# Kernel tuning notes

Hardware: AMD Instinct MI355X
Metric: run time of the kernel (lower is better)

Reference implementation:

```python
import jax, jax.numpy as jnp
import numpy as np


def conv2d(x, w, b, stride=1, pad=0):
    out = jax.lax.conv_general_dilated(
        x, w, (stride, stride), ((pad, pad), (pad, pad)),
        dimension_numbers=('NCHW', 'OIHW', 'NCHW'))
    return out + b[None, :, None, None]


def maxpool2(x):
    return jax.lax.reduce_window(x, -jnp.inf, jax.lax.max,
                                 (1, 1, 2, 2), (1, 1, 2, 2), 'VALID')


def pixel_match_(x, y):
    # x, y: (1, C, H, W). 9-way shifted squared-diff cost volume.
    _, C, H, W = x.shape
    yc = y[0, :, 1:H - 1, 1:W - 1]
    inner = []
    for dh in range(3):
        for dw in range(3):
            tmp = x[0, :, dh:dh + H - 2, dw:dw + W - 2] - yc
            inner.append(jnp.sum(tmp * tmp, axis=0))
    inner = jnp.stack(inner)  # (9, H-2, W-2)
    diff = jnp.zeros((9, H, W), x.dtype).at[:, 1:H - 1, 1:W - 1].set(inner)
    diff = 1.0 / jnp.sqrt(diff + 0.01)
    diff = diff / jnp.sum(diff, axis=0, keepdims=True)
    return diff[None]  # (1, 9, H, W)


def positional(H, W, dtype):
    h = jnp.arange(H, dtype=dtype)
    w = jnp.arange(W, dtype=dtype)
    h = 2.0 * h / h[-1] - 1.0
    w = 2.0 * w / w[-1] - 1.0
    ph = jnp.broadcast_to(h[:, None], (H, W))
    pw = jnp.broadcast_to(w[None, :], (H, W))
    return jnp.stack([ph, pw])[None]  # (1, 2, H, W)


def pixel_match(x, y):
    return jnp.concatenate(
        [pixel_match_(x, y), pixel_match_(y, x),
         positional(x.shape[2], x.shape[3], x.dtype)], axis=1)


def adaptive_max_pool3(x):
    # torch adaptive_max_pool2d semantics: bin i spans [floor(i*H/3), ceil((i+1)*H/3))
    _, C, H, W = x.shape
    rows = []
    for i in range(3):
        hs, he = (i * H) // 3, -((-(i + 1) * H) // 3)
        cols = []
        for j in range(3):
            ws, we = (j * W) // 3, -((-(j + 1) * W) // 3)
            cols.append(jnp.max(x[:, :, hs:he, ws:we], axis=(2, 3)))
        rows.append(jnp.stack(cols, axis=-1))
    return jnp.stack(rows, axis=-2)  # (1, C, 3, 3)


def setup_inputs() -> dict:
    key = jax.random.key(0)
    ks = jax.random.split(key, 16)
    f = jnp.float32
    H = W = 1024
    s = 0.05
    return {
        'x1': jax.random.normal(ks[0], (3, H, W), f),
        'x2': jax.random.normal(ks[1], (3, H, W), f),
        'enc_w': jax.random.normal(ks[2], (24, 3, 3, 3), f) * s,
        'enc_b': jax.random.normal(ks[3], (24,), f) * s,
        'embed_w': jax.random.normal(ks[4], (32, 24, 1, 1), f) * s,
        'embed_b': jax.random.normal(ks[5], (32,), f) * s,
        'dense_w': jax.random.normal(ks[6], (8, 32, 5, 5), f) * s,
        'dense_b': jax.random.normal(ks[7], (8,), f) * s,
        'f1_w': jax.random.normal(ks[8], (64, 48, 1, 1), f) * s,
        'f1_b': jax.random.normal(ks[9], (64,), f) * s,
        'f2_w': jax.random.normal(ks[10], (128, 64, 3, 3), f) * s,
        'f2_b': jax.random.normal(ks[11], (128,), f) * s,
        'f3_w': jax.random.normal(ks[12], (6, 128), f) * s,
        'f3_b': jax.random.normal(ks[13], (6,), f) * s,
    }


def reference(x1, x2, enc_w, enc_b, embed_w, embed_b, dense_w, dense_b,
              f1_w, f1_b, f2_w, f2_b, f3_w, f3_b):
    def coding(x):
        x = x[None]  # (1,3,H,W)
        x = jax.lax.stop_gradient(conv2d(x, enc_w, enc_b, pad=1))  # frozen encoder
        x = conv2d(x, embed_w, embed_b)
        return maxpool2(x)

    c1 = coding(x1)
    c2 = coding(x2)
    level1 = maxpool2(pixel_match(c1, c2))
    p1 = maxpool2(c1)
    p2 = maxpool2(c2)
    level2 = pixel_match(p1, p2)
    dense = jax.nn.leaky_relu(conv2d(p1 - p2, dense_w, dense_b, pad=2))
    x = jnp.concatenate([level1, level2, dense], axis=1)  # (1,48,H/4,W/4)
    x = conv2d(x, f1_w, f1_b)
    x = adaptive_max_pool3(x)
    x = conv2d(x, f2_w, f2_b).reshape(1, 128)
    tmp = jnp.sum(x * x) + 0.001
    x = x / jnp.sqrt(tmp)
    x = (x @ f3_w.T + f3_b).reshape(2, 3)
    x = jnp.concatenate([x, jnp.zeros((1, 3), x.dtype)], axis=0)
    return jnp.eye(3, dtype=x.dtype) + jnp.clip(x, -0.11, 0.11) + x * 0.01
```

## Files before the change

### kernel.cpp

```cpp
#include <hip/hip_runtime.h>
#include <math.h>


__global__ void fuse_weights_kernel(const float* __restrict__ enc_w,
                                    const float* __restrict__ enc_b,
                                    const float* __restrict__ embed_w,
                                    const float* __restrict__ embed_b,
                                    float* __restrict__ weff_t,
                                    float* __restrict__ beff) {
    int t = threadIdx.x;
    for (int idx = t; idx < 27 * 32; idx += blockDim.x) {
        int r = idx >> 5, o = idx & 31;
        float s = 0.f;
        for (int k = 0; k < 24; ++k) s += embed_w[o * 24 + k] * enc_w[k * 27 + r];
        weff_t[idx] = s;
    }
    if (t < 32) {
        float s = embed_b[t];
        for (int k = 0; k < 24; ++k) s += embed_w[t * 24 + k] * enc_b[k];
        beff[t] = s;
    }
}

__global__ __launch_bounds__(256) void coding_kernel(
    const float* __restrict__ x1, const float* __restrict__ x2,
    const float* __restrict__ weff_t, const float* __restrict__ beff,
    float* __restrict__ c1, float* __restrict__ c2,
    float* __restrict__ p1, float* __restrict__ p2) {
    int tx = threadIdx.x, ty = threadIdx.y;
    int img = blockIdx.z;
    const float* x = img ? x2 : x1;
    float* c = img ? c2 : c1;
    float* p = img ? p2 : p1;
    int Y = blockIdx.y * 16 + ty;
    int cx = blockIdx.x * 16 + tx;
    int X0 = 2 * cx;
    bool interior = (blockIdx.y > 0 && blockIdx.y < 63 &&
                     blockIdx.x > 0 && blockIdx.x < 31);
    float acc0[32], acc1[32];
#pragma unroll
    for (int o = 0; o < 32; ++o) {
        acc0[o] = beff[o];
        acc1[o] = acc0[o];
    }
#pragma unroll 1
    for (int ci = 0; ci < 3; ++ci) {
        float in[3][4];
        const float* xc = x + ci * 1048576;
        if (interior) {
#pragma unroll
            for (int r = 0; r < 3; ++r) {
                const float* row = xc + (Y - 1 + r) * 1024 + X0 - 1;
#pragma unroll
                for (int q = 0; q < 4; ++q) in[r][q] = row[q];
            }
        } else {
#pragma unroll
            for (int r = 0; r < 3; ++r)
#pragma unroll
                for (int q = 0; q < 4; ++q) {
                    int gy = Y - 1 + r, gx = X0 - 1 + q;
                    in[r][q] = (gy >= 0 && gy < 1024 && gx >= 0 && gx < 1024)
                                   ? xc[gy * 1024 + gx]
                                   : 0.f;
                }
        }
#pragma unroll
        for (int ky = 0; ky < 3; ++ky)
#pragma unroll
            for (int kx = 0; kx < 3; ++kx) {
                const float* wrow = weff_t + (ci * 9 + ky * 3 + kx) * 32;
                float xa = in[ky][kx];
                float xb = in[ky][kx + 1];
#pragma unroll
                for (int o = 0; o < 32; ++o) {
                    float wv = wrow[o];
                    acc0[o] = fmaf(wv, xa, acc0[o]);
                    acc1[o] = fmaf(wv, xb, acc1[o]);
                }
            }
    }
#pragma unroll
    for (int o = 0; o < 32; ++o) {
        float m = fmaxf(acc0[o], acc1[o]);
        acc0[o] = fmaxf(m, __shfl_xor(m, 16, 64));
    }
    int cpix = (Y >> 1) * 512 + cx;
    if ((ty & 1) == 0) {
        float4* cd = (float4*)(c + cpix * 32);
#pragma unroll
        for (int q = 0; q < 8; ++q)
            cd[q] = make_float4(acc0[4 * q], acc0[4 * q + 1], acc0[4 * q + 2],
                                acc0[4 * q + 3]);
    }
#pragma unroll
    for (int o = 0; o < 32; ++o) {
        float v = fmaxf(acc0[o], __shfl_xor(acc0[o], 1, 64));
        acc0[o] = fmaxf(v, __shfl_xor(v, 32, 64));
    }
    if (((ty & 3) == 0) && ((tx & 1) == 0)) {
        int ppix = (Y >> 2) * 256 + (cx >> 1);
        float4* pd = (float4*)(p + ppix * 32);
#pragma unroll
        for (int q = 0; q < 8; ++q)
            pd[q] = make_float4(acc0[4 * q], acc0[4 * q + 1], acc0[4 * q + 2],
                                acc0[4 * q + 3]);
    }
}

__global__ __launch_bounds__(256) void pm512_pool_kernel(
    const float* __restrict__ c1, const float* __restrict__ c2,
    float* __restrict__ feat) {
    int tid = threadIdx.x;
    int quad = tid & 3;
    int pl = tid >> 2;
    int px = pl & 7, py = pl >> 3;
    int sw = blockIdx.x * 8 + px;
    int sh = blockIdx.y * 8 + py;
    bool interior = (sh >= 1 && sh <= 510 && sw >= 1 && sw <= 510);
    const float* b1 = c1 + (sh * 512 + sw) * 32 + quad * 8;
    const float* b2 = c2 + (sh * 512 + sw) * 32 + quad * 8;
    float a1[9], a2[9];
#pragma unroll
    for (int k = 0; k < 9; ++k) { a1[k] = 0.f; a2[k] = 0.f; }
    if (interior) {
        float4 y1a = ((const float4*)b1)[0], y1b = ((const float4*)b1)[1];
        float4 y2a = ((const float4*)b2)[0], y2b = ((const float4*)b2)[1];
#pragma unroll
        for (int dh = -1; dh <= 1; ++dh)
#pragma unroll
            for (int dw = -1; dw <= 1; ++dw) {
                int k = (dh + 1) * 3 + (dw + 1);
                const float4* n1 = (const float4*)(b1 + (dh * 512 + dw) * 32);
                const float4* n2 = (const float4*)(b2 + (dh * 512 + dw) * 32);
                float4 na = n1[0], nA = n1[1], nb = n2[0], nB = n2[1];
                float s1 = a1[k], s2 = a2[k], t;
                t = na.x - y2a.x; s1 = fmaf(t, t, s1);
                t = na.y - y2a.y; s1 = fmaf(t, t, s1);
                t = na.z - y2a.z; s1 = fmaf(t, t, s1);
                t = na.w - y2a.w; s1 = fmaf(t, t, s1);
                t = nA.x - y2b.x; s1 = fmaf(t, t, s1);
                t = nA.y - y2b.y; s1 = fmaf(t, t, s1);
                t = nA.z - y2b.z; s1 = fmaf(t, t, s1);
                t = nA.w - y2b.w; s1 = fmaf(t, t, s1);
                t = nb.x - y1a.x; s2 = fmaf(t, t, s2);
                t = nb.y - y1a.y; s2 = fmaf(t, t, s2);
                t = nb.z - y1a.z; s2 = fmaf(t, t, s2);
                t = nb.w - y1a.w; s2 = fmaf(t, t, s2);
                t = nB.x - y1b.x; s2 = fmaf(t, t, s2);
                t = nB.y - y1b.y; s2 = fmaf(t, t, s2);
                t = nB.z - y1b.z; s2 = fmaf(t, t, s2);
                t = nB.w - y1b.w; s2 = fmaf(t, t, s2);
                a1[k] = s1;
                a2[k] = s2;
            }
    }
#pragma unroll
    for (int k = 0; k < 9; ++k) {
        a1[k] += __shfl_xor(a1[k], 1, 64);
        a1[k] += __shfl_xor(a1[k], 2, 64);
        a2[k] += __shfl_xor(a2[k], 1, 64);
        a2[k] += __shfl_xor(a2[k], 2, 64);
    }
    float d[20];
    if (interior) {
        float s1 = 0.f, s2 = 0.f;
#pragma unroll
        for (int k = 0; k < 9; ++k) {
            a1[k] = 1.0f / sqrtf(a1[k] + 0.01f);
            a2[k] = 1.0f / sqrtf(a2[k] + 0.01f);
            s1 += a1[k];
            s2 += a2[k];
        }
        float i1 = 1.0f / s1, i2 = 1.0f / s2;
#pragma unroll
        for (int k = 0; k < 9; ++k) {
            d[k] = a1[k] * i1;
            d[9 + k] = a2[k] * i2;
        }
    } else {
#pragma unroll
        for (int k = 0; k < 18; ++k) d[k] = 1.0f / 9.0f;
    }
#pragma unroll
    for (int k = 0; k < 18; ++k) {
        float v = fmaxf(d[k], __shfl_xor(d[k], 4, 64));
        d[k] = fmaxf(v, __shfl_xor(v, 32, 64));
    }
    d[18] = 2.0f * (sh | 1) / 511.0f - 1.0f;
    d[19] = 2.0f * (sw | 1) / 511.0f - 1.0f;
    if ((tid & 36) == 0) {
        int opix = (sh >> 1) * 256 + (sw >> 1);
#pragma unroll
        for (int j = 0; j < 5; ++j)
            feat[(quad * 5 + j) * 65536 + opix] = d[quad * 5 + j];
    }
}

__global__ __launch_bounds__(256) void pm256_kernel(
    const float* __restrict__ p1, const float* __restrict__ p2,
    float* __restrict__ feat) {
    int tid = threadIdx.x;
    int quad = tid & 3;
    int pl = tid >> 2;
    int px = pl & 7, py = pl >> 3;
    int w = blockIdx.x * 8 + px;
    int h = blockIdx.y * 8 + py;
    bool interior = (h >= 1 && h <= 254 && w >= 1 && w <= 254);
    const float* b1 = p1 + (h * 256 + w) * 32 + quad * 8;
    const float* b2 = p2 + (h * 256 + w) * 32 + quad * 8;
    float a1[9], a2[9];
#pragma unroll
    for (int k = 0; k < 9; ++k) { a1[k] = 0.f; a2[k] = 0.f; }
    if (interior) {
        float4 y1a = ((const float4*)b1)[0], y1b = ((const float4*)b1)[1];
        float4 y2a = ((const float4*)b2)[0], y2b = ((const float4*)b2)[1];
#pragma unroll
        for (int dh = -1; dh <= 1; ++dh)
#pragma unroll
            for (int dw = -1; dw <= 1; ++dw) {
                int k = (dh + 1) * 3 + (dw + 1);
                const float4* n1 = (const float4*)(b1 + (dh * 256 + dw) * 32);
                const float4* n2 = (const float4*)(b2 + (dh * 256 + dw) * 32);
                float4 na = n1[0], nA = n1[1], nb = n2[0], nB = n2[1];
                float s1 = a1[k], s2 = a2[k], t;
                t = na.x - y2a.x; s1 = fmaf(t, t, s1);
                t = na.y - y2a.y; s1 = fmaf(t, t, s1);
                t = na.z - y2a.z; s1 = fmaf(t, t, s1);
                t = na.w - y2a.w; s1 = fmaf(t, t, s1);
                t = nA.x - y2b.x; s1 = fmaf(t, t, s1);
                t = nA.y - y2b.y; s1 = fmaf(t, t, s1);
                t = nA.z - y2b.z; s1 = fmaf(t, t, s1);
                t = nA.w - y2b.w; s1 = fmaf(t, t, s1);
                t = nb.x - y1a.x; s2 = fmaf(t, t, s2);
                t = nb.y - y1a.y; s2 = fmaf(t, t, s2);
                t = nb.z - y1a.z; s2 = fmaf(t, t, s2);
                t = nb.w - y1a.w; s2 = fmaf(t, t, s2);
                t = nB.x - y1b.x; s2 = fmaf(t, t, s2);
                t = nB.y - y1b.y; s2 = fmaf(t, t, s2);
                t = nB.z - y1b.z; s2 = fmaf(t, t, s2);
                t = nB.w - y1b.w; s2 = fmaf(t, t, s2);
                a1[k] = s1;
                a2[k] = s2;
            }
    }
#pragma unroll
    for (int k = 0; k < 9; ++k) {
        a1[k] += __shfl_xor(a1[k], 1, 64);
        a1[k] += __shfl_xor(a1[k], 2, 64);
        a2[k] += __shfl_xor(a2[k], 1, 64);
        a2[k] += __shfl_xor(a2[k], 2, 64);
    }
    float d[20];
    if (interior) {
        float s1 = 0.f, s2 = 0.f;
#pragma unroll
        for (int k = 0; k < 9; ++k) {
            a1[k] = 1.0f / sqrtf(a1[k] + 0.01f);
            a2[k] = 1.0f / sqrtf(a2[k] + 0.01f);
            s1 += a1[k];
            s2 += a2[k];
        }
        float i1 = 1.0f / s1, i2 = 1.0f / s2;
#pragma unroll
        for (int k = 0; k < 9; ++k) {
            d[k] = a1[k] * i1;
            d[9 + k] = a2[k] * i2;
        }
    } else {
#pragma unroll
        for (int k = 0; k < 18; ++k) d[k] = 1.0f / 9.0f;
    }
    d[18] = 2.0f * h / 255.0f - 1.0f;
    d[19] = 2.0f * w / 255.0f - 1.0f;
    int pix = h * 256 + w;
#pragma unroll
    for (int j = 0; j < 5; ++j)
        feat[(20 + quad * 5 + j) * 65536 + pix] = d[quad * 5 + j];
}

__global__ __launch_bounds__(256) void dense_part_kernel(
    const float* __restrict__ p1, const float* __restrict__ p2,
    const float* __restrict__ dw, float* __restrict__ part) {
    __shared__ float sdiff[4 * 1296];
    __shared__ float sw[4 * 8 * 28];
    int tx = threadIdx.x, ty = threadIdx.y;
    int tid = ty * 16 + tx;
    int bz = blockIdx.z;
    int h0 = blockIdx.y * 32, w0 = blockIdx.x * 32;
    for (int idx = tid; idx < 1296; idx += 256) {
        int yy = idx / 36, xx = idx % 36;
        int gy = h0 + yy - 2, gx = w0 + xx - 2;
        float4 dv = make_float4(0.f, 0.f, 0.f, 0.f);
        if (gy >= 0 && gy < 256 && gx >= 0 && gx < 256) {
            const float4* q1 =
                (const float4*)(p1 + (gy * 256 + gx) * 32 + bz * 4);
            const float4* q2 =
                (const float4*)(p2 + (gy * 256 + gx) * 32 + bz * 4);
            float4 v1 = q1[0], v2 = q2[0];
            dv = make_float4(v1.x - v2.x, v1.y - v2.y, v1.z - v2.z, v1.w - v2.w);
        }
        sdiff[0 * 1296 + idx] = dv.x;
        sdiff[1 * 1296 + idx] = dv.y;
        sdiff[2 * 1296 + idx] = dv.z;
        sdiff[3 * 1296 + idx] = dv.w;
    }
    for (int idx = tid; idx < 4 * 8 * 28; idx += 256) {
        int ci = idx / 224, r = idx % 224;
        int o = r / 28, k = r % 28;
        sw[idx] = (k < 25) ? dw[o * 800 + (bz * 4 + ci) * 25 + k] : 0.f;
    }
    __syncthreads();
    float acc[4][8];
#pragma unroll
    for (int pq = 0; pq < 4; ++pq)
#pragma unroll
        for (int o = 0; o < 8; ++o) acc[pq][o] = 0.f;
    for (int ci = 0; ci < 4; ++ci) {
        float patch[6][6];
#pragma unroll
        for (int yy = 0; yy < 6; ++yy) {
            const float* rowp = &sdiff[ci * 1296 + (2 * ty + yy) * 36 + 2 * tx];
#pragma unroll
            for (int cpair = 0; cpair < 3; ++cpair) {
                float2 lp = *(const float2*)&rowp[2 * cpair];
                patch[yy][2 * cpair] = lp.x;
                patch[yy][2 * cpair + 1] = lp.y;
            }
        }
#pragma unroll
        for (int o = 0; o < 8; ++o) {
            float wreg[28];
            const float4* wp = (const float4*)&sw[(ci * 8 + o) * 28];
#pragma unroll
            for (int q = 0; q < 7; ++q) {
                float4 wv = wp[q];
                wreg[4 * q] = wv.x;
                wreg[4 * q + 1] = wv.y;
                wreg[4 * q + 2] = wv.z;
                wreg[4 * q + 3] = wv.w;
            }
#pragma unroll
            for (int ky = 0; ky < 5; ++ky)
#pragma unroll
                for (int kx = 0; kx < 5; ++kx) {
                    float wv = wreg[ky * 5 + kx];
#pragma unroll
                    for (int pq = 0; pq < 4; ++pq)
                        acc[pq][o] = fmaf(
                            wv, patch[ky + (pq >> 1)][kx + (pq & 1)], acc[pq][o]);
                }
        }
    }
#pragma unroll
    for (int pq = 0; pq < 4; ++pq) {
        int h = h0 + 2 * ty + (pq >> 1), w = w0 + 2 * tx + (pq & 1);
        int pix = h * 256 + w;
#pragma unroll
        for (int o = 0; o < 8; ++o)
            part[bz * 524288 + o * 65536 + pix] = acc[pq][o];
    }
}

__global__ __launch_bounds__(256) void dense_reduce_kernel(
    const float* __restrict__ part, const float* __restrict__ db,
    float* __restrict__ feat) {
    int idx = blockIdx.x * 256 + threadIdx.x;
    int o = idx >> 16;
    float s = db[o];
#pragma unroll
    for (int z = 0; z < 8; ++z) s += part[z * 524288 + idx];
    float v = (s >= 0.f) ? s : 0.01f * s;
    feat[40 * 65536 + idx] = v;
}

__global__ __launch_bounds__(256) void f1_kernel(
    const float* __restrict__ feat, const float* __restrict__ f1w,
    const float* __restrict__ f1b, float* __restrict__ out) {
    __shared__ float sw[1536];
    __shared__ float sb[32];
    int og = blockIdx.y;
    int tid = threadIdx.x;
    for (int i = tid; i < 1536; i += 256) sw[i] = f1w[og * 1536 + i];
    if (tid < 32) sb[tid] = f1b[og * 32 + tid];
    __syncthreads();
    int pix = blockIdx.x * 256 + tid;
    float f[48];
#pragma unroll
    for (int c = 0; c < 48; ++c) f[c] = feat[c * 65536 + pix];
#pragma unroll
    for (int o = 0; o < 32; ++o) {
        float a = sb[o];
        const float4* wv = (const float4*)&sw[o * 48];
#pragma unroll
        for (int c4 = 0; c4 < 12; ++c4) {
            float4 ww = wv[c4];
            a = fmaf(ww.x, f[c4 * 4], a);
            a = fmaf(ww.y, f[c4 * 4 + 1], a);
            a = fmaf(ww.z, f[c4 * 4 + 2], a);
            a = fmaf(ww.w, f[c4 * 4 + 3], a);
        }
        out[(og * 32 + o) * 65536 + pix] = a;
    }
}

__global__ __launch_bounds__(256) void pool3_kernel(
    const float* __restrict__ f1out, float* __restrict__ pooled) {
    int b = blockIdx.x;
    int c = b / 9, ij = b % 9, i = ij / 3, j = ij % 3;
    int hs = (i * 256) / 3, he = ((i + 1) * 256 + 2) / 3;
    int ws = (j * 256) / 3, we = ((j + 1) * 256 + 2) / 3;
    const float* src = f1out + c * 65536;
    int nh = he - hs, nw = we - ws, tot = nh * nw;
    float m = -INFINITY;
    for (int t = threadIdx.x; t < tot; t += 256) {
        int r = t / nw, q = t - r * nw;
        m = fmaxf(m, src[(hs + r) * 256 + (ws + q)]);
    }
    for (int off = 32; off > 0; off >>= 1) m = fmaxf(m, __shfl_down(m, off, 64));
    __shared__ float red[4];
    if ((threadIdx.x & 63) == 0) red[threadIdx.x >> 6] = m;
    __syncthreads();
    if (threadIdx.x == 0)
        pooled[b] = fmaxf(fmaxf(red[0], red[1]), fmaxf(red[2], red[3]));
}

__global__ __launch_bounds__(128) void final_kernel(
    const float* __restrict__ pooled, const float* __restrict__ f2w,
    const float* __restrict__ f2b, const float* __restrict__ f3w,
    const float* __restrict__ f3b, float* __restrict__ out) {
    __shared__ float xn[128];
    __shared__ float red[2];
    __shared__ float ov[6];
    int t = threadIdx.x;
    float a = f2b[t];
    for (int c = 0; c < 64; ++c)
#pragma unroll
        for (int k = 0; k < 9; ++k)
            a = fmaf(f2w[t * 576 + c * 9 + k], pooled[c * 9 + k], a);
    float sq = a * a;
    for (int off = 32; off > 0; off >>= 1) sq += __shfl_down(sq, off, 64);
    if ((t & 63) == 0) red[t >> 6] = sq;
    __syncthreads();
    float tmp = red[0] + red[1] + 0.001f;
    float scale = 1.0f / sqrtf(tmp);
    xn[t] = a * scale;
    __syncthreads();
    if (t < 6) {
        float o = f3b[t];
        for (int k = 0; k < 128; ++k) o = fmaf(f3w[t * 128 + k], xn[k], o);
        ov[t] = o;
    }
    __syncthreads();
    if (t < 9) {
        int r = t / 3, cc = t % 3;
        float v = 0.f;
        if (r < 2) {
            float x = ov[r * 3 + cc];
            float cl = fminf(fmaxf(x, -0.11f), 0.11f);
            v = cl + 0.01f * x;
        }
        if (r == cc) v += 1.0f;
        out[t] = v;
    }
}

extern "C" void kernel_launch(void* const* d_in, const int* in_sizes, int n_in,
                              void* d_out, int out_size, void* d_ws,
                              size_t ws_size, hipStream_t stream) {
    const float* x1 = (const float*)d_in[0];
    const float* x2 = (const float*)d_in[1];
    const float* enc_w = (const float*)d_in[2];
    const float* enc_b = (const float*)d_in[3];
    const float* embed_w = (const float*)d_in[4];
    const float* embed_b = (const float*)d_in[5];
    const float* dense_w = (const float*)d_in[6];
    const float* dense_b = (const float*)d_in[7];
    const float* f1_w = (const float*)d_in[8];
    const float* f1_b = (const float*)d_in[9];
    const float* f2_w = (const float*)d_in[10];
    const float* f2_b = (const float*)d_in[11];
    const float* f3_w = (const float*)d_in[12];
    const float* f3_b = (const float*)d_in[13];

    float* ws = (float*)d_ws;
    float* weff_t = ws;
    float* beff = ws + 864;
    float* c1 = ws + 1024;
    float* c2 = c1 + 8388608;
    float* p1 = c2 + 8388608;
    float* p2 = p1 + 2097152;
    float* feat = p2 + 2097152;
    float* pooled = feat + 3145728;
    float* f1o = c1;
    float* part = c2;

    fuse_weights_kernel<<<1, 256, 0, stream>>>(enc_w, enc_b, embed_w, embed_b,
                                               weff_t, beff);
    coding_kernel<<<dim3(32, 64, 2), dim3(16, 16), 0, stream>>>(
        x1, x2, weff_t, beff, c1, c2, p1, p2);
    pm512_pool_kernel<<<dim3(64, 64), 256, 0, stream>>>(c1, c2, feat);
    pm256_kernel<<<dim3(32, 32), 256, 0, stream>>>(p1, p2, feat);
    dense_part_kernel<<<dim3(8, 8, 8), dim3(16, 16), 0, stream>>>(
        p1, p2, dense_w, part);
    dense_reduce_kernel<<<2048, 256, 0, stream>>>(part, dense_b, feat);
    f1_kernel<<<dim3(256, 2), 256, 0, stream>>>(feat, f1_w, f1_b, f1o);
    pool3_kernel<<<576, 256, 0, stream>>>(f1o, pooled);
    final_kernel<<<1, 128, 0, stream>>>(pooled, f2_w, f2_b, f3_w, f3_b,
                                        (float*)d_out);
}
```

Measured before the change: 184.9 us.

## Split coding conv channels across lanes and read weights directly from global

The coding kernel now gives each pooled pixel to four lanes, each computing 8 output channels over a 2x2 window instead of 32 channels for two pixels. This cuts per-thread accumulator registers and lets each lane write contiguous float4 chunks without the first shuffle stage. The dense and f1 kernels drop their shared-memory weight staging and read the uniform weights straight from global memory, with rolled loops to limit code size and registers. This relies on scalar/constant caching of the weights and may raise the number of global loads per FMA.

Result: slower. 213.4 us (+15.4%).

```diff
diff --git a/kernel.cpp b/kernel.cpp
--- a/kernel.cpp
+++ b/kernel.cpp
@@ -27,39 +27,46 @@
     const float* __restrict__ weff_t, const float* __restrict__ beff,
     float* __restrict__ c1, float* __restrict__ c2,
     float* __restrict__ p1, float* __restrict__ p2) {
-    int tx = threadIdx.x, ty = threadIdx.y;
+    int tid = threadIdx.x;
+    int quad = tid & 3;
+    int pl = tid >> 2;
+    int px = pl & 7, py = pl >> 3;
     int img = blockIdx.z;
     const float* x = img ? x2 : x1;
     float* c = img ? c2 : c1;
     float* p = img ? p2 : p1;
-    int Y = blockIdx.y * 16 + ty;
-    int cx = blockIdx.x * 16 + tx;
-    int X0 = 2 * cx;
+    int cy = blockIdx.y * 8 + py;
+    int cx = blockIdx.x * 8 + px;
+    int Y0 = 2 * cy, X0 = 2 * cx;
     bool interior = (blockIdx.y > 0 && blockIdx.y < 63 &&
-                     blockIdx.x > 0 && blockIdx.x < 31);
-    float acc0[32], acc1[32];
-#pragma unroll
-    for (int o = 0; o < 32; ++o) {
-        acc0[o] = beff[o];
-        acc1[o] = acc0[o];
+                     blockIdx.x > 0 && blockIdx.x < 63);
+    float4 bb0 = *(const float4*)(beff + quad * 8);
+    float4 bb1 = *(const float4*)(beff + quad * 8 + 4);
+    float acc[4][8];
+#pragma unroll
+    for (int pos = 0; pos < 4; ++pos) {
+        acc[pos][0] = bb0.x; acc[pos][1] = bb0.y;
+        acc[pos][2] = bb0.z; acc[pos][3] = bb0.w;
+        acc[pos][4] = bb1.x; acc[pos][5] = bb1.y;
+        acc[pos][6] = bb1.z; acc[pos][7] = bb1.w;
     }
 #pragma unroll 1
     for (int ci = 0; ci < 3; ++ci) {
-        float in[3][4];
+        float in[4][4];
         const float* xc = x + ci * 1048576;
         if (interior) {
 #pragma unroll
-            for (int r = 0; r < 3; ++r) {
-                const float* row = xc + (Y - 1 + r) * 1024 + X0 - 1;
+            for (int r = 0; r < 4; ++r) {
+                const float* row = xc + (Y0 - 1 + r) * 1024 + X0 - 1;
 #pragma unroll
                 for (int q = 0; q < 4; ++q) in[r][q] = row[q];
             }
         } else {
 #pragma unroll
-            for (int r = 0; r < 3; ++r)
+            for (int r = 0; r < 4; ++r)
 #pragma unroll
                 for (int q = 0; q < 4; ++q) {
-                    int gy = Y - 1 + r, gx = X0 - 1 + q;
+                    int gy = Y0 - 1 + r, gx = X0 - 1 + q;
                     in[r][q] = (gy >= 0 && gy < 1024 && gx >= 0 && gx < 1024)
                                    ? xc[gy * 1024 + gx]
                                    : 0.f;
@@ -69,42 +76,42 @@
         for (int ky = 0; ky < 3; ++ky)
 #pragma unroll
             for (int kx = 0; kx < 3; ++kx) {
-                const float* wrow = weff_t + (ci * 9 + ky * 3 + kx) * 32;
-                float xa = in[ky][kx];
-                float xb = in[ky][kx + 1];
-#pragma unroll
-                for (int o = 0; o < 32; ++o) {
-                    float wv = wrow[o];
-                    acc0[o] = fmaf(wv, xa, acc0[o]);
-                    acc1[o] = fmaf(wv, xb, acc1[o]);
+                const float4* wp = (const float4*)(weff_t +
+                                                   (ci * 9 + ky * 3 + kx) * 32 +
+                                                   quad * 8);
+                float4 w0 = wp[0], w1 = wp[1];
+#pragma unroll
+                for (int pos = 0; pos < 4; ++pos) {
+                    float xv = in[(pos >> 1) + ky][(pos & 1) + kx];
+                    acc[pos][0] = fmaf(w0.x, xv, acc[pos][0]);
+                    acc[pos][1] = fmaf(w0.y, xv, acc[pos][1]);
+                    acc[pos][2] = fmaf(w0.z, xv, acc[pos][2]);
+                    acc[pos][3] = fmaf(w0.w, xv, acc[pos][3]);
+                    acc[pos][4] = fmaf(w1.x, xv, acc[pos][4]);
+                    acc[pos][5] = fmaf(w1.y, xv, acc[pos][5]);
+                    acc[pos][6] = fmaf(w1.z, xv, acc[pos][6]);
+                    acc[pos][7] = fmaf(w1.w, xv, acc[pos][7]);
                 }
             }
     }
-#pragma unroll
-    for (int o = 0; o < 32; ++o) {
-        float m = fmaxf(acc0[o], acc1[o]);
-        acc0[o] = fmaxf(m, __shfl_xor(m, 16, 64));
-    }
-    int cpix = (Y >> 1) * 512 + cx;
-    if ((ty & 1) == 0) {
-        float4* cd = (float4*)(c + cpix * 32);
-#pragma unroll
-        for (int q = 0; q < 8; ++q)
-            cd[q] = make_float4(acc0[4 * q], acc0[4 * q + 1], acc0[4 * q + 2],
-                                acc0[4 * q + 3]);
-    }
-#pragma unroll
-    for (int o = 0; o < 32; ++o) {
-        float v = fmaxf(acc0[o], __shfl_xor(acc0[o], 1, 64));
-        acc0[o] = fmaxf(v, __shfl_xor(v, 32, 64));
-    }
-    if (((ty & 3) == 0) && ((tx & 1) == 0)) {
-        int ppix = (Y >> 2) * 256 + (cx >> 1);
-        float4* pd = (float4*)(p + ppix * 32);
-#pragma unroll
-        for (int q = 0; q < 8; ++q)
-            pd[q] = make_float4(acc0[4 * q], acc0[4 * q + 1], acc0[4 * q + 2],
-                                acc0[4 * q + 3]);
+    float m[8];
+#pragma unroll
+    for (int o = 0; o < 8; ++o)
+        m[o] = fmaxf(fmaxf(acc[0][o], acc[1][o]), fmaxf(acc[2][o], acc[3][o]));
+    int cpix = cy * 512 + cx;
+    float4* cd = (float4*)(c + cpix * 32 + quad * 8);
+    cd[0] = make_float4(m[0], m[1], m[2], m[3]);
+    cd[1] = make_float4(m[4], m[5], m[6], m[7]);
+#pragma unroll
+    for (int o = 0; o < 8; ++o) {
+        float v = fmaxf(m[o], __shfl_xor(m[o], 4, 64));
+        m[o] = fmaxf(v, __shfl_xor(v, 32, 64));
+    }
+    if ((tid & 36) == 0) {
+        int ppix = (cy >> 1) * 256 + (cx >> 1);
+        float4* pd = (float4*)(p + ppix * 32 + quad * 8);
+        pd[0] = make_float4(m[0], m[1], m[2], m[3]);
+        pd[1] = make_float4(m[4], m[5], m[6], m[7]);
     }
 }
 
@@ -283,7 +290,6 @@
     const float* __restrict__ p1, const float* __restrict__ p2,
     const float* __restrict__ dw, float* __restrict__ part) {
     __shared__ float sdiff[4 * 1296];
-    __shared__ float sw[4 * 8 * 28];
     int tx = threadIdx.x, ty = threadIdx.y;
     int tid = ty * 16 + tx;
     int bz = blockIdx.z;
@@ -305,17 +311,13 @@
         sdiff[2 * 1296 + idx] = dv.z;
         sdiff[3 * 1296 + idx] = dv.w;
     }
-    for (int idx = tid; idx < 4 * 8 * 28; idx += 256) {
-        int ci = idx / 224, r = idx % 224;
-        int o = r / 28, k = r % 28;
-        sw[idx] = (k < 25) ? dw[o * 800 + (bz * 4 + ci) * 25 + k] : 0.f;
-    }
     __syncthreads();
     float acc[4][8];
 #pragma unroll
     for (int pq = 0; pq < 4; ++pq)
 #pragma unroll
         for (int o = 0; o < 8; ++o) acc[pq][o] = 0.f;
+#pragma unroll 1
     for (int ci = 0; ci < 4; ++ci) {
         float patch[6][6];
 #pragma unroll
@@ -328,23 +330,14 @@
                 patch[yy][2 * cpair + 1] = lp.y;
             }
         }
-#pragma unroll
+#pragma unroll 1
         for (int o = 0; o < 8; ++o) {
-            float wreg[28];
-            const float4* wp = (const float4*)&sw[(ci * 8 + o) * 28];
-#pragma unroll
-            for (int q = 0; q < 7; ++q) {
-                float4 wv = wp[q];
-                wreg[4 * q] = wv.x;
-                wreg[4 * q + 1] = wv.y;
-                wreg[4 * q + 2] = wv.z;
-                wreg[4 * q + 3] = wv.w;
-            }
+            const float* wrow = dw + o * 800 + (bz * 4 + ci) * 25;
 #pragma unroll
             for (int ky = 0; ky < 5; ++ky)
 #pragma unroll
                 for (int kx = 0; kx < 5; ++kx) {
-                    float wv = wreg[ky * 5 + kx];
+                    float wv = wrow[ky * 5 + kx];
 #pragma unroll
                     for (int pq = 0; pq < 4; ++pq)
                         acc[pq][o] = fmaf(
@@ -377,30 +370,20 @@
 __global__ __launch_bounds__(256) void f1_kernel(
     const float* __restrict__ feat, const float* __restrict__ f1w,
     const float* __restrict__ f1b, float* __restrict__ out) {
-    __shared__ float sw[1536];
-    __shared__ float sb[32];
     int og = blockIdx.y;
     int tid = threadIdx.x;
-    for (int i = tid; i < 1536; i += 256) sw[i] = f1w[og * 1536 + i];
-    if (tid < 32) sb[tid] = f1b[og * 32 + tid];
-    __syncthreads();
     int pix = blockIdx.x * 256 + tid;
     float f[48];
 #pragma unroll
     for (int c = 0; c < 48; ++c) f[c] = feat[c * 65536 + pix];
-#pragma unroll
+#pragma unroll 1
     for (int o = 0; o < 32; ++o) {
-        float a = sb[o];
-        const float4* wv = (const float4*)&sw[o * 48];
-#pragma unroll
-        for (int c4 = 0; c4 < 12; ++c4) {
-            float4 ww = wv[c4];
-            a = fmaf(ww.x, f[c4 * 4], a);
-            a = fmaf(ww.y, f[c4 * 4 + 1], a);
-            a = fmaf(ww.z, f[c4 * 4 + 2], a);
-            a = fmaf(ww.w, f[c4 * 4 + 3], a);
-        }
-        out[(og * 32 + o) * 65536 + pix] = a;
+        int oo = og * 32 + o;
+        const float* wr = f1w + oo * 48;
+        float a = f1b[oo];
+#pragma unroll
+        for (int c = 0; c < 48; ++c) a = fmaf(wr[c], f[c], a);
+        out[oo * 65536 + pix] = a;
     }
 }
 
@@ -497,7 +480,7 @@
 
     fuse_weights_kernel<<<1, 256, 0, stream>>>(enc_w, enc_b, embed_w, embed_b,
                                                weff_t, beff);
-    coding_kernel<<<dim3(32, 64, 2), dim3(16, 16), 0, stream>>>(
+    coding_kernel<<<dim3(64, 64, 2), 256, 0, stream>>>(
         x1, x2, weff_t, beff, c1, c2, p1, p2);
     pm512_pool_kernel<<<dim3(64, 64), 256, 0, stream>>>(c1, c2, feat);
     pm256_kernel<<<dim3(32, 32), 256, 0, stream>>>(p1, p2, feat);
```

## Fuse f1 1x1 conv with row-wise adaptive max pooling via shared memory

Applied to the files above, without the earlier changes.

The f1 1x1 convolution now keeps its per-row outputs in shared memory and reduces them straight into three column-bin maxima per row, instead of writing the full 64x256x256 map to global memory and reading it back in a separate pool kernel. A small second kernel then reduces the row partials over the row bins. This removes about 16 MB of write plus read traffic. In exchange it uses a large shared-memory tile (about 37 KB) that may limit occupancy, reads weights from global/scalar memory instead of an LDS copy, and does the column reduction serially on only 96 threads.

Result: slower. 195.8 us (+5.9%).

```diff
diff --git a/kernel.cpp b/kernel.cpp
--- a/kernel.cpp
+++ b/kernel.cpp
@@ -374,55 +374,53 @@
     feat[40 * 65536 + idx] = v;
 }
 
-__global__ __launch_bounds__(256) void f1_kernel(
+__global__ __launch_bounds__(256) void f1_pool_kernel(
     const float* __restrict__ feat, const float* __restrict__ f1w,
-    const float* __restrict__ f1b, float* __restrict__ out) {
-    __shared__ float sw[1536];
-    __shared__ float sb[32];
+    const float* __restrict__ f1b, float* __restrict__ rowpart) {
+    __shared__ float lt[256 * 37];
     int og = blockIdx.y;
-    int tid = threadIdx.x;
-    for (int i = tid; i < 1536; i += 256) sw[i] = f1w[og * 1536 + i];
-    if (tid < 32) sb[tid] = f1b[og * 32 + tid];
+    int w = threadIdx.x;
+    int h = blockIdx.x;
+    int pix = h * 256 + w;
+    float f[48];
+#pragma unroll
+    for (int c = 0; c < 48; ++c) f[c] = feat[c * 65536 + pix];
+#pragma unroll 2
+    for (int o = 0; o < 32; ++o) {
+        int oo = og * 32 + o;
+        const float* wr = f1w + oo * 48;
+        float a = f1b[oo];
+#pragma unroll
+        for (int c = 0; c < 48; ++c) a = fmaf(wr[c], f[c], a);
+        lt[w * 37 + o] = a;
+    }
     __syncthreads();
-    int pix = blockIdx.x * 256 + tid;
-    float f[48];
-#pragma unroll
-    for (int c = 0; c < 48; ++c) f[c] = feat[c * 65536 + pix];
-#pragma unroll
-    for (int o = 0; o < 32; ++o) {
-        float a = sb[o];
-        const float4* wv = (const float4*)&sw[o * 48];
-#pragma unroll
-        for (int c4 = 0; c4 < 12; ++c4) {
-            float4 ww = wv[c4];
-            a = fmaf(ww.x, f[c4 * 4], a);
-            a = fmaf(ww.y, f[c4 * 4 + 1], a);
-            a = fmaf(ww.z, f[c4 * 4 + 2], a);
-            a = fmaf(ww.w, f[c4 * 4 + 3], a);
-        }
-        out[(og * 32 + o) * 65536 + pix] = a;
-    }
-}
-
-__global__ __launch_bounds__(256) void pool3_kernel(
-    const float* __restrict__ f1out, float* __restrict__ pooled) {
-    int b = blockIdx.x;
-    int c = b / 9, ij = b % 9, i = ij / 3, j = ij % 3;
+    int t = threadIdx.x;
+    if (t < 96) {
+        int r = t >> 5, o = t & 31;
+        const int ws0[3] = {0, 85, 170};
+        const int we0[3] = {86, 171, 256};
+        float m = -INFINITY;
+        for (int ww = ws0[r]; ww < we0[r]; ++ww)
+            m = fmaxf(m, lt[ww * 37 + o]);
+        rowpart[h * 192 + r * 64 + og * 32 + o] = m;
+    }
+}
+
+__global__ __launch_bounds__(256) void pool3b_kernel(
+    const float* __restrict__ rowpart, float* __restrict__ pooled) {
+    int j = blockIdx.x, i = blockIdx.y;
+    int ch = threadIdx.x & 63, ck = threadIdx.x >> 6;
     int hs = (i * 256) / 3, he = ((i + 1) * 256 + 2) / 3;
-    int ws = (j * 256) / 3, we = ((j + 1) * 256 + 2) / 3;
-    const float* src = f1out + c * 65536;
-    int nh = he - hs, nw = we - ws, tot = nh * nw;
     float m = -INFINITY;
-    for (int t = threadIdx.x; t < tot; t += 256) {
-        int r = t / nw, q = t - r * nw;
-        m = fmaxf(m, src[(hs + r) * 256 + (ws + q)]);
-    }
-    for (int off = 32; off > 0; off >>= 1) m = fmaxf(m, __shfl_down(m, off, 64));
-    __shared__ float red[4];
-    if ((threadIdx.x & 63) == 0) red[threadIdx.x >> 6] = m;
+    for (int h = hs + ck; h < he; h += 4)
+        m = fmaxf(m, rowpart[h * 192 + j * 64 + ch]);
+    __shared__ float red[4][64];
+    red[ck][ch] = m;
     __syncthreads();
-    if (threadIdx.x == 0)
-        pooled[b] = fmaxf(fmaxf(red[0], red[1]), fmaxf(red[2], red[3]));
+    if (ck == 0)
+        pooled[ch * 9 + i * 3 + j] =
+            fmaxf(fmaxf(red[0][ch], red[1][ch]), fmaxf(red[2][ch], red[3][ch]));
 }
 
 __global__ __launch_bounds__(128) void final_kernel(
@@ -492,7 +490,7 @@
     float* p2 = p1 + 2097152;
     float* feat = p2 + 2097152;
     float* pooled = feat + 3145728;
-    float* f1o = c1;
+    float* rowpart = pooled + 576;
     float* part = c2;
 
     fuse_weights_kernel<<<1, 256, 0, stream>>>(enc_w, enc_b, embed_w, embed_b,
@@ -504,8 +502,8 @@
     dense_part_kernel<<<dim3(8, 8, 8), dim3(16, 16), 0, stream>>>(
         p1, p2, dense_w, part);
     dense_reduce_kernel<<<2048, 256, 0, stream>>>(part, dense_b, feat);
-    f1_kernel<<<dim3(256, 2), 256, 0, stream>>>(feat, f1_w, f1_b, f1o);
-    pool3_kernel<<<576, 256, 0, stream>>>(f1o, pooled);
+    f1_pool_kernel<<<dim3(256, 2), 256, 0, stream>>>(feat, f1_w, f1_b, rowpart);
+    pool3b_kernel<<<dim3(3, 3), 256, 0, stream>>>(rowpart, pooled);
     final_kernel<<<1, 128, 0, stream>>>(pooled, f2_w, f2_b, f3_w, f3_b,
                                         (float*)d_out);
 }
```
